# Kernel optimization log

Hardware: AMD Instinct MI355X
Metric: run time of the kernel (lower is better)

## Reference

```python
import jax, jax.numpy as jnp
import numpy as np
from jax import lax

LPC_ORDER = 24  # M, even -> even-order branch
LOG_GAIN = False


def roots_to_poly(r):
    """Monic polynomial coefficients from roots r[..., n].

    Matches diffsptk RootsToPolynomial: c starts as [1,0,...,0] and for each
    root c[1:m+2] -= r_m * c[0:m+1], i.e. c <- c - r * shift_right(c).
    Returns coeffs of shape (..., n+1), descending powers, leading 1.
    """
    n = r.shape[-1]
    c0 = jnp.zeros(r.shape[:-1] + (n + 1,), dtype=r.dtype).at[..., 0].set(1.0)

    def step(c, rt):
        shifted = jnp.concatenate([jnp.zeros_like(c[..., :1]), c[..., :-1]], axis=-1)
        return c - rt[..., None] * shifted, None

    c, _ = lax.scan(step, c0, jnp.moveaxis(r, -1, 0))
    return c


def setup_inputs() -> dict:
    key = jax.random.key(0)
    # LSP frequencies in radians live in (0, pi); uniform [0,1) is in-range.
    w = jax.random.uniform(key, (512, 2048, LPC_ORDER + 1), dtype=jnp.float32)
    return {"w": w}


def reference(w):
    M = LPC_ORDER
    K = w[..., :1]
    if LOG_GAIN:
        K = jnp.exp(K)
    ang = w[..., 1:]                       # (..., M)
    z = jnp.exp(1j * ang.astype(jnp.complex64))
    p_r = z[..., 1::2]                     # (..., M//2)
    q_r = z[..., 0::2]                     # (..., M//2)
    # roots come in conjugate pairs -> real polynomials
    P = roots_to_poly(jnp.concatenate([p_r, jnp.conj(p_r)], axis=-1)).real  # (..., M+1)
    Q = roots_to_poly(jnp.concatenate([q_r, jnp.conj(q_r)], axis=-1)).real  # (..., M+1)
    # conv1d (cross-correlation) with kernel_p=[-1,1], kernel_q=[1,1], no padding (even M)
    p_c = P[..., 1:] - P[..., :-1]         # (..., M)
    q_c = Q[..., :-1] + Q[..., 1:]         # (..., M)
    a = 0.5 * (p_c + q_c)
    return jnp.concatenate([K, a], axis=-1)
```

## Files before the change

### kernel.cpp

```cpp
#include <hip/hip_runtime.h>


typedef float f4 __attribute__((ext_vector_type(4)));
typedef float f2 __attribute__((ext_vector_type(2)));

static constexpr int NC   = 25;
static constexpr int RPW  = 64;
static constexpr int FPW  = NC * RPW;
static constexpr int V4W  = FPW / 4;
static constexpr int TAIL = V4W - 6 * 64;

__global__ __launch_bounds__(256)
void lsp2lpc_kernel(const float* __restrict__ in, float* __restrict__ out) {
    __shared__ float lds[4 * FPW];
    const int tid  = threadIdx.x;
    const int wid  = tid >> 6;
    const int lane = tid & 63;

    float* chunk = &lds[wid * FPW];
    f4*    c4    = reinterpret_cast<f4*>(chunk);

    const int tile = blockIdx.x * 4 + wid;
    const size_t base = (size_t)tile * FPW;

    const f4* gin = reinterpret_cast<const f4*>(in + base);
#pragma unroll
    for (int i = 0; i < 6; ++i)
        c4[lane + i * 64] = gin[lane + i * 64];
    if (lane < TAIL)
        c4[lane + 6 * 64] = gin[lane + 6 * 64];

    const float* row = &chunk[lane * NC];
    const float K = row[0];
    f2 tcoef[12];
#pragma unroll
    for (int m = 0; m < 12; ++m) {
        const float cq = __cosf(row[1 + 2 * m]);
        const float cp = __cosf(row[2 + 2 * m]);
        tcoef[m] = (f2){-2.f * cp, -2.f * cq};
    }

    f2 PQ[13];
#pragma unroll
    for (int k = 0; k < 13; ++k) PQ[k] = (f2){0.f, 0.f};
    PQ[0] = (f2){1.f, 1.f};

#pragma unroll
    for (int m = 0; m < 12; ++m) {
        const f2 tm = tcoef[m];
        const int kmax = (2 * m + 2 < 12) ? (2 * m + 2) : 12;
#pragma unroll
        for (int k = 12; k >= 0; --k) {
            if (k > kmax) continue;
            const f2 c1 = (k >= 1) ? PQ[k - 1] : (f2){0.f, 0.f};
            const f2 c2 = (k >= 2) ? PQ[k - 2] : (f2){0.f, 0.f};
            PQ[k] = __builtin_elementwise_fma(tm, c1, PQ[k]) + c2;
        }
    }

    float u[13], v[13];
#pragma unroll
    for (int k = 0; k < 13; ++k) {
        u[k] = PQ[k].x + PQ[k].y;
        v[k] = PQ[k].y - PQ[k].x;
    }
    float* orow = &chunk[lane * NC];
    orow[0] = K;
#pragma unroll
    for (int k = 0; k < 24; ++k) {
        const int i0 = (k     <= 12) ? k       : 24 - k;
        const int i1 = (k + 1 <= 12) ? (k + 1) : 24 - (k + 1);
        orow[1 + k] = 0.5f * (u[i1] + v[i0]);
    }

    f4* gout = reinterpret_cast<f4*>(out + base);
#pragma unroll
    for (int i = 0; i < 6; ++i)
        __builtin_nontemporal_store(c4[lane + i * 64], &gout[lane + i * 64]);
    if (lane < TAIL)
        __builtin_nontemporal_store(c4[lane + 6 * 64], &gout[lane + 6 * 64]);
}

extern "C" void kernel_launch(void* const* d_in, const int* in_sizes, int n_in,
                              void* d_out, int out_size, void* d_ws, size_t ws_size,
                              hipStream_t stream) {
    const float* in  = (const float*)d_in[0];
    float*       out = (float*)d_out;
    const int nrows   = in_sizes[0] / NC;
    const int ntiles  = nrows / RPW;
    const int nblocks = ntiles / 4;
    lsp2lpc_kernel<<<nblocks, 256, 0, stream>>>(in, out);
}
```

Before: 37.88 us.

## Split P and Q polynomial expansion across lane pairs with DPP exchange

```diff
diff --git a/kernel.cpp b/kernel.cpp
--- a/kernel.cpp
+++ b/kernel.cpp
@@ -2,15 +2,19 @@
 
 
 typedef float f4 __attribute__((ext_vector_type(4)));
-typedef float f2 __attribute__((ext_vector_type(2)));
 
 static constexpr int NC   = 25;
-static constexpr int RPW  = 64;
+static constexpr int RPW  = 32;
 static constexpr int FPW  = NC * RPW;
 static constexpr int V4W  = FPW / 4;
-static constexpr int TAIL = V4W - 6 * 64;
 
-__global__ __launch_bounds__(256)
+__device__ __forceinline__ float xor1(float x) {
+    int i = __float_as_int(x);
+    i = __builtin_amdgcn_mov_dpp(i, 0xB1, 0xF, 0xF, true);
+    return __int_as_float(i);
+}
+
+__global__ __launch_bounds__(256, 8)
 void lsp2lpc_kernel(const float* __restrict__ in, float* __restrict__ out) {
     __shared__ float lds[4 * FPW];
     const int tid  = threadIdx.x;
@@ -25,60 +29,67 @@
 
     const f4* gin = reinterpret_cast<const f4*>(in + base);
 #pragma unroll
-    for (int i = 0; i < 6; ++i)
+    for (int i = 0; i < 3; ++i)
         c4[lane + i * 64] = gin[lane + i * 64];
-    if (lane < TAIL)
-        c4[lane + 6 * 64] = gin[lane + 6 * 64];
+    if (lane < V4W - 192)
+        c4[lane + 192] = gin[lane + 192];
 
-    const float* row = &chunk[lane * NC];
+    const int lrow = lane >> 1;
+    const int p    = lane & 1;
+    const float* row = &chunk[lrow * NC];
     const float K = row[0];
-    f2 tcoef[12];
+
+    float t[12];
+#pragma unroll
+    for (int m = 0; m < 12; ++m)
+        t[m] = -2.f * __cosf(row[1 + p + 2 * m]);
+
+    float c[13];
+    c[0] = 1.f;
+#pragma unroll
+    for (int k = 1; k < 13; ++k) c[k] = 0.f;
 #pragma unroll
     for (int m = 0; m < 12; ++m) {
-        const float cq = __cosf(row[1 + 2 * m]);
-        const float cp = __cosf(row[2 + 2 * m]);
-        tcoef[m] = (f2){-2.f * cp, -2.f * cq};
-    }
-
-    f2 PQ[13];
-#pragma unroll
-    for (int k = 0; k < 13; ++k) PQ[k] = (f2){0.f, 0.f};
-    PQ[0] = (f2){1.f, 1.f};
-
-#pragma unroll
-    for (int m = 0; m < 12; ++m) {
-        const f2 tm = tcoef[m];
+        const float tm = t[m];
         const int kmax = (2 * m + 2 < 12) ? (2 * m + 2) : 12;
 #pragma unroll
-        for (int k = 12; k >= 0; --k) {
+        for (int k = 12; k >= 1; --k) {
             if (k > kmax) continue;
-            const f2 c1 = (k >= 1) ? PQ[k - 1] : (f2){0.f, 0.f};
-            const f2 c2 = (k >= 2) ? PQ[k - 2] : (f2){0.f, 0.f};
-            PQ[k] = __builtin_elementwise_fma(tm, c1, PQ[k]) + c2;
+            const float c1 = c[k - 1];
+            const float c2 = (k >= 2) ? c[k - 2] : 0.f;
+            c[k] = fmaf(tm, c1, c[k]) + c2;
         }
     }
 
-    float u[13], v[13];
+    float u[13], d[13];
 #pragma unroll
     for (int k = 0; k < 13; ++k) {
-        u[k] = PQ[k].x + PQ[k].y;
-        v[k] = PQ[k].y - PQ[k].x;
+        const float pc = xor1(c[k]);
+        u[k] = 0.5f * (c[k] + pc);
+        d[k] = 0.5f * (c[k] - pc);
     }
-    float* orow = &chunk[lane * NC];
-    orow[0] = K;
+
+    float* orow = &chunk[lrow * NC];
+    if (p == 0) {
+        orow[0] = K;
 #pragma unroll
-    for (int k = 0; k < 24; ++k) {
-        const int i0 = (k     <= 12) ? k       : 24 - k;
-        const int i1 = (k + 1 <= 12) ? (k + 1) : 24 - (k + 1);
-        orow[1 + k] = 0.5f * (u[i1] + v[i0]);
+        for (int k = 0; k < 12; ++k)
+            orow[1 + k] = u[k + 1] + d[k];
+    } else {
+#pragma unroll
+        for (int k = 12; k < 24; ++k) {
+            const int i0 = (k <= 12) ? k : 24 - k;
+            const int i1 = 23 - k + 0;
+            orow[1 + k] = u[i1] - d[i0];
+        }
     }
 
     f4* gout = reinterpret_cast<f4*>(out + base);
 #pragma unroll
-    for (int i = 0; i < 6; ++i)
+    for (int i = 0; i < 3; ++i)
         __builtin_nontemporal_store(c4[lane + i * 64], &gout[lane + i * 64]);
-    if (lane < TAIL)
-        __builtin_nontemporal_store(c4[lane + 6 * 64], &gout[lane + 6 * 64]);
+    if (lane < V4W - 192)
+        __builtin_nontemporal_store(c4[lane + 192], &gout[lane + 192]);
 }
 
 extern "C" void kernel_launch(void* const* d_in, const int* in_sizes, int n_in,
```

New measurement: 37.45 us. Within noise of the previous version (-1.1%).
